# Kernel tuning notes

Measured on AMD Instinct MI355X. Metric: run time of the kernel, lower is better.

Reference implementation:

```python
import jax, jax.numpy as jnp
import numpy as np

B, S, D, H, DFF = 2, 2048, 1024, 16, 4096
HD = D // H
EPS = 1e-5


def setup_inputs() -> dict:
    key = jax.random.key(0)
    ks = jax.random.split(key, 8)
    s = lambda fan_in: 1.0 / np.sqrt(fan_in)
    return {
        "x": jax.random.normal(ks[0], (B, S, D), jnp.float32),
        "ln1_g": jnp.ones((D,), jnp.float32),
        "ln1_b": jnp.zeros((D,), jnp.float32),
        "Wq": jax.random.normal(ks[1], (D, D), jnp.float32) * s(D),
        "Wk": jax.random.normal(ks[2], (D, D), jnp.float32) * s(D),
        "Wv": jax.random.normal(ks[3], (D, D), jnp.float32) * s(D),
        "Wo": jax.random.normal(ks[4], (D, D), jnp.float32) * s(D),
        "bo": jnp.zeros((D,), jnp.float32),
        "ln2_g": jnp.ones((D,), jnp.float32),
        "ln2_b": jnp.zeros((D,), jnp.float32),
        "W1": jax.random.normal(ks[5], (D, DFF), jnp.float32) * s(D),
        "b1": jnp.zeros((DFF,), jnp.float32),
        "W2": jax.random.normal(ks[6], (DFF, D), jnp.float32) * s(DFF),
        "b2": jnp.zeros((D,), jnp.float32),
    }


def _layernorm(x, g, b):
    mu = jnp.mean(x, axis=-1, keepdims=True)
    var = jnp.var(x, axis=-1, keepdims=True)
    return (x - mu) * jax.lax.rsqrt(var + EPS) * g + b


def reference(x, ln1_g, ln1_b, Wq, Wk, Wv, Wo, bo, ln2_g, ln2_b, W1, b1, W2, b2):
    # --- pre-LN + causal multi-head attention + residual ---
    h = _layernorm(x, ln1_g, ln1_b)
    q = (h @ Wq).reshape(B, S, H, HD).transpose(0, 2, 1, 3)  # [B,H,S,hd]
    k = (h @ Wk).reshape(B, S, H, HD).transpose(0, 2, 1, 3)
    v = (h @ Wv).reshape(B, S, H, HD).transpose(0, 2, 1, 3)
    scores = jnp.einsum("bhqd,bhkd->bhqk", q, k) / jnp.sqrt(jnp.float32(HD))
    causal = jnp.triu(jnp.ones((S, S), bool), k=1)  # True above diagonal -> masked
    scores = jnp.where(causal, -jnp.inf, scores)
    attn = jax.nn.softmax(scores, axis=-1)  # dropout is identity at inference
    ctx = jnp.einsum("bhqk,bhkd->bhqd", attn, v)
    ctx = ctx.transpose(0, 2, 1, 3).reshape(B, S, D)
    x = x + ctx @ Wo + bo
    # --- pre-LN + MLP + residual ---
    h = _layernorm(x, ln2_g, ln2_b)
    h = jax.nn.gelu(h @ W1 + b1, approximate=False)  # torch nn.GELU default = exact
    x = x + h @ W2 + b2
    return x
```

## Files before the change

kernel.cpp:

```cpp
#include <hip/hip_runtime.h>
#include <hip/hip_bf16.h>
#include <math.h>

using bf16 = __hip_bfloat16;
typedef short bf16x8 __attribute__((ext_vector_type(8)));
typedef float f32x4 __attribute__((ext_vector_type(4)));

static constexpr int B = 2, S = 2048, D = 1024, H = 16, HD = 64, DFF = 4096;
static constexpr int NR = B * S;
static constexpr int DQ = 3072;
static constexpr float EPS = 1e-5f;

__device__ __forceinline__ bf16 f2b(float v) { return __float2bfloat16(v); }

__device__ __forceinline__ float gelu_exact(float v) {
    const float u = v * 0.70710678118654752f;
    const float au = fabsf(u);
    const float t = __builtin_amdgcn_rcpf(1.0f + 0.3275911f * au);
    float poly = 1.061405429f;
    poly = poly * t - 1.453152027f;
    poly = poly * t + 1.421413741f;
    poly = poly * t - 0.284496736f;
    poly = poly * t + 0.254829592f;
    poly = poly * t;
    const float ea = 1.0f - poly * __expf(-u * u);
    return 0.5f * v * (1.0f + copysignf(ea, u));
}

typedef __attribute__((address_space(1))) const void* gp1_t;
typedef __attribute__((address_space(3))) void* sp3_t;
__device__ __forceinline__ void gld_lds16(const bf16* g, bf16* l) {
    __builtin_amdgcn_global_load_lds((gp1_t)(const void*)g, (sp3_t)(void*)l, 16, 0, 0);
}

__device__ __forceinline__ void convT_body(const float* __restrict__ src,
                                           bf16* __restrict__ dst,
                                           int K, int N, int k0, int n0, int tid) {
    __shared__ float tile[64][65];
    const int r = tid >> 4, c = (tid & 15) * 4;
#pragma unroll
    for (int rr = 0; rr < 64; rr += 16) {
        float4 v = *(const float4*)&src[(size_t)(k0 + r + rr) * N + n0 + c];
        tile[r + rr][c] = v.x; tile[r + rr][c + 1] = v.y;
        tile[r + rr][c + 2] = v.z; tile[r + rr][c + 3] = v.w;
    }
    __syncthreads();
    const int n = tid >> 2, ks = (tid & 3) * 16;
    union { bf16 h[16]; int4 v2[2]; } o;
#pragma unroll
    for (int i = 0; i < 16; ++i) o.h[i] = f2b(tile[ks + i][n]);
    bf16* dp = &dst[(size_t)(n0 + n) * K + k0 + ks];
    *(int4*)dp = o.v2[0];
    *(int4*)(dp + 8) = o.v2[1];
}

__global__ __launch_bounds__(256) void convT_kernel(const float* __restrict__ src,
                                                    bf16* __restrict__ dst,
                                                    int K, int N) {
    convT_body(src, dst, K, N, blockIdx.x * 64, blockIdx.y * 64, threadIdx.x);
}

__global__ __launch_bounds__(256) void convT6_kernel(const float* __restrict__ Wq,
                                                     const float* __restrict__ Wk,
                                                     const float* __restrict__ Wv,
                                                     const float* __restrict__ Wo,
                                                     const float* __restrict__ W2,
                                                     const float* __restrict__ W1,
                                                     bf16* __restrict__ WqkvT,
                                                     bf16* __restrict__ WoT,
                                                     bf16* __restrict__ W2T,
                                                     bf16* __restrict__ W1T) {
    const int bid = blockIdx.x;
    const float* src;
    bf16* dst;
    int K, N, bx, by;
    if (bid < 768) {
        const int j = bid >> 8, r = bid & 255;
        src = (j == 0) ? Wq : ((j == 1) ? Wk : Wv);
        dst = WqkvT + (size_t)j * D * D;
        K = D; N = D; bx = r & 15; by = r >> 4;
    } else if (bid < 1024) {
        const int r = bid - 768;
        src = Wo; dst = WoT; K = D; N = D; bx = r & 15; by = r >> 4;
    } else if (bid < 2048) {
        const int r = bid - 1024;
        src = W2; dst = W2T; K = DFF; N = D; bx = r & 63; by = r >> 6;
    } else {
        const int r = bid - 2048;
        src = W1; dst = W1T; K = D; N = DFF; bx = r & 15; by = r >> 4;
    }
    convT_body(src, dst, K, N, bx * 64, by * 64, threadIdx.x);
}

__global__ __launch_bounds__(256) void ln_kernel(const float* __restrict__ x,
                                                 const float* __restrict__ g,
                                                 const float* __restrict__ b,
                                                 bf16* __restrict__ out) {
    const int row = blockIdx.x;
    const int tid = threadIdx.x;
    const float4 v4 = ((const float4*)(x + (size_t)row * D))[tid];
    float v[4] = {v4.x, v4.y, v4.z, v4.w};
    float s = v[0] + v[1] + v[2] + v[3];
    float sq = v[0] * v[0] + v[1] * v[1] + v[2] * v[2] + v[3] * v[3];
#pragma unroll
    for (int off = 32; off >= 1; off >>= 1) {
        s += __shfl_xor(s, off);
        sq += __shfl_xor(sq, off);
    }
    __shared__ float ssum[4], ssq[4];
    const int wave = tid >> 6;
    if ((tid & 63) == 0) { ssum[wave] = s; ssq[wave] = sq; }
    __syncthreads();
    s = ssum[0] + ssum[1] + ssum[2] + ssum[3];
    sq = ssq[0] + ssq[1] + ssq[2] + ssq[3];
    const float mu = s * (1.0f / D);
    const float var = sq * (1.0f / D) - mu * mu;
    const float rstd = rsqrtf(var + EPS);
    bf16* orow = out + (size_t)row * D;
#pragma unroll
    for (int i = 0; i < 4; ++i) {
        const int c = tid * 4 + i;
        orow[c] = f2b((v[i] - mu) * rstd * g[c] + b[c]);
    }
}

template <int EPI, int BN, int TPB>
__global__ __launch_bounds__(256) void gemm_bt(const bf16* __restrict__ A,
                                               const bf16* __restrict__ Bt,
                                               const float* __restrict__ bias,
                                               const float* __restrict__ res,
                                               void* __restrict__ Cv,
                                               int M, int N, int K) {
    constexpr int NTW = BN / 32;
    constexpr int AHALF = 128 * 32;
    constexpr int BHALF = BN * 32;
    constexpr int ASZ = 2 * AHALF, BSZ = 2 * BHALF;
    constexpr int CST = BN + 8;
    __shared__ __align__(16) bf16 smem[2 * (ASZ + BSZ)];

    const int Mtiles = M / 128;
    const int p = blockIdx.x;
    const int tm = p % Mtiles;
    const int tn0 = (p / Mtiles) * TPB;
    const int tid = threadIdx.x;
    const int wave = tid >> 6, lane = tid & 63;
    const int wm = wave >> 1, wn = wave & 1;
    const int quad = lane >> 4, l16 = lane & 15;

    const int r4 = tid >> 2, s4 = (tid & 3) * 8;
    const size_t K64 = (size_t)64 * K;
    const int nk = K / 64;

    for (int tp = 0; tp < TPB; ++tp) {
        const int tn = tn0 + tp;
        if (tp) __syncthreads();

        f32x4 acc[4][NTW];
#pragma unroll
        for (int i = 0; i < 4; ++i)
#pragma unroll
            for (int j = 0; j < NTW; ++j) acc[i][j] = (f32x4){0.f, 0.f, 0.f, 0.f};

        const bf16* Ap = A + (size_t)(tm * 128 + r4) * K + s4;
        const bf16* Bp = Bt + (size_t)(tn * BN + r4) * K + s4;

        gld_lds16(Ap, smem + tid * 8);
        gld_lds16(Ap + K64, smem + (256 + tid) * 8);
        gld_lds16(Ap + 32, smem + (512 + tid) * 8);
        gld_lds16(Ap + K64 + 32, smem + (768 + tid) * 8);
        gld_lds16(Bp, smem + 2 * ASZ + tid * 8);
        gld_lds16(Bp + 32, smem + 2 * ASZ + (256 + tid) * 8);
        Ap += 64;
        Bp += 64;

        for (int kt = 0; kt < nk; ++kt) {
            const int cur = kt & 1, nxt = cur ^ 1;
            bf16* Acur = smem + cur * ASZ;
            bf16* Bcur = smem + 2 * ASZ + cur * BSZ;
            __syncthreads();
            if (kt + 1 < nk) {
                bf16* Anxt = smem + nxt * ASZ;
                bf16* Bnxt = smem + 2 * ASZ + nxt * BSZ;
                gld_lds16(Ap, Anxt + tid * 8);
                gld_lds16(Ap + K64, Anxt + (256 + tid) * 8);
                gld_lds16(Ap + 32, Anxt + (512 + tid) * 8);
                gld_lds16(Ap + K64 + 32, Anxt + (768 + tid) * 8);
                gld_lds16(Bp, Bnxt + tid * 8);
                gld_lds16(Bp + 32, Bnxt + (256 + tid) * 8);
                Ap += 64;
                Bp += 64;
            }

#pragma unroll
            for (int ks = 0; ks < 2; ++ks) {
                const bf16* Ah = Acur + ks * AHALF;
                const bf16* Bh = Bcur + ks * BHALF;
                bf16x8 aF[4], bF[NTW];
#pragma unroll
                for (int mt = 0; mt < 4; ++mt)
                    aF[mt] = *(const bf16x8*)(Ah + (wm * 64 + mt * 16 + l16) * 32 + quad * 8);
#pragma unroll
                for (int nt = 0; nt < NTW; ++nt)
                    bF[nt] = *(const bf16x8*)(Bh + (wn * (BN / 2) + nt * 16 + l16) * 32 + quad * 8);
#pragma unroll
                for (int mt = 0; mt < 4; ++mt)
#pragma unroll
                    for (int nt = 0; nt < NTW; ++nt)
                        acc[mt][nt] = __builtin_amdgcn_mfma_f32_16x16x32_bf16(
                            aF[mt], bF[nt], acc[mt][nt], 0, 0, 0);
            }
        }

        if constexpr (EPI == 1) {
#pragma unroll
            for (int nt = 0; nt < NTW; ++nt) {
                const int col = tn * BN + wn * (BN / 2) + nt * 16 + l16;
                const float bv = bias[col];
#pragma unroll
                for (int mt = 0; mt < 4; ++mt) {
                    const int row0 = tm * 128 + wm * 64 + mt * 16 + quad * 4;
#pragma unroll
                    for (int j = 0; j < 4; ++j) {
                        const size_t idx = (size_t)(row0 + j) * N + col;
                        ((float*)Cv)[idx] = acc[mt][nt][j] + bv + res[idx];
                    }
                }
            }
        } else {
            bf16* C = (bf16*)Cv;
            __syncthreads();
#pragma unroll
            for (int nt = 0; nt < NTW; ++nt) {
                const int ccol = wn * (BN / 2) + nt * 16 + l16;
                float bv = 0.f;
                if (EPI == 2) bv = bias[tn * BN + ccol];
#pragma unroll
                for (int mt = 0; mt < 4; ++mt) {
                    const int r0 = wm * 64 + mt * 16 + quad * 4;
#pragma unroll
                    for (int j = 0; j < 4; ++j) {
                        float v = acc[mt][nt][j];
                        if (EPI == 2) v = gelu_exact(v + bv);
                        smem[(r0 + j) * CST + ccol] = f2b(v);
                    }
                }
            }
            __syncthreads();
            bf16* crow = C + (size_t)(tm * 128) * N + tn * BN;
#pragma unroll
            for (int i = 0; i < BN / 16; ++i) {
                const int gid = i * 256 + tid;
                const int row = gid / (BN / 8), c8 = gid % (BN / 8);
                const int4 val = *(const int4*)(smem + row * CST + c8 * 8);
                *(int4*)(crow + (size_t)row * N + c8 * 8) = val;
            }
        }
    }
}

__global__ __launch_bounds__(256) void fattn_kernel(const bf16* __restrict__ QKV,
                                                    bf16* __restrict__ ctx) {
    const int id = blockIdx.x;
    const int bh = id & 31;
    const int k = id >> 5;
    const int t = (k < 16) ? 31 - k : k - 16;
    const int b = bh >> 4, h = bh & (H - 1);
    const int tid = threadIdx.x;
    const int wave = tid >> 6, lane = tid & 63;
    const int quad = lane >> 4, l16 = lane & 15;
    const bf16* Qp = QKV + (size_t)b * S * DQ + h * HD;
    const bf16* Kp = Qp + D;
    const bf16* Vp = Qp + 2 * D;

    __shared__ __align__(16) bf16 Ks[2][64 * 64];
    __shared__ __align__(16) bf16 Vt[2][64][72];

    const int keyA = tid >> 3;
    const int sA = (keyA & 3) | ((keyA >> 1) & 4);
    const int dsA = ((tid & 7) ^ sA) * 8;
    const size_t K32 = (size_t)32 * DQ;

    const int q0 = t * 64;
    const bf16* qg = Qp + (size_t)(q0 + wave * 16 + l16) * DQ + quad * 8;
    union U8 { bf16 h[8]; bf16x8 v; };
    U8 uq0, uq1;
    uq0.v = *(const bf16x8*)(qg);
    uq1.v = *(const bf16x8*)(qg + 32);
#pragma unroll
    for (int i = 0; i < 8; ++i) {
        uq0.h[i] = f2b(__bfloat162float(uq0.h[i]) * 0.125f);
        uq1.h[i] = f2b(__bfloat162float(uq1.h[i]) * 0.125f);
    }
    const bf16x8 aQ0 = uq0.v;
    const bf16x8 aQ1 = uq1.v;

    const int kb = (l16 >> 2) * 8 + (l16 & 3);
    const int sQ = (l16 & 3) | (((l16 >> 2) & 1) << 2);
    const int ofs0 = kb * 64 + ((quad ^ sQ) * 8);
    const int ofs1 = kb * 64 + (((4 + quad) ^ sQ) * 8);

    f32x4 O[4];
#pragma unroll
    for (int nt = 0; nt < 4; ++nt) O[nt] = (f32x4){0.f, 0.f, 0.f, 0.f};
    float rowm = -3.0e38f, rowl = 0.f;

    gld_lds16(Kp + (size_t)keyA * DQ + dsA, Ks[0] + tid * 8);
    gld_lds16(Kp + K32 + (size_t)keyA * DQ + dsA, Ks[0] + (256 + tid) * 8);
    {
        const bf16* vg = Vp + (size_t)lane * DQ + wave * 16;
        U8 u0, u1;
        u0.v = *(const bf16x8*)vg;
        u1.v = *(const bf16x8*)(vg + 8);
#pragma unroll
        for (int i = 0; i < 8; ++i) {
            Vt[0][wave * 16 + i][lane] = u0.h[i];
            Vt[0][wave * 16 + 8 + i][lane] = u1.h[i];
        }
    }

    const int nch = t + 1;
    for (int c = 0; c < nch; ++c) {
        const int cur = c & 1, nxt = cur ^ 1;
        __syncthreads();
        U8 u0, u1;
        if (c + 1 < nch) {
            const bf16* kg = Kp + (size_t)((c + 1) * 64 + keyA) * DQ + dsA;
            gld_lds16(kg, Ks[nxt] + tid * 8);
            gld_lds16(kg + K32, Ks[nxt] + (256 + tid) * 8);
            const bf16* vg = Vp + (size_t)((c + 1) * 64 + lane) * DQ + wave * 16;
            u0.v = *(const bf16x8*)vg;
            u1.v = *(const bf16x8*)(vg + 8);
        }

        f32x4 sc[4];
        __builtin_amdgcn_s_setprio(1);
#pragma unroll
        for (int m = 0; m < 4; ++m) {
            const bf16* kr = Ks[cur] + (m & 1) * 256 + (m >> 1) * 2048;
            const bf16x8 bK0 = *(const bf16x8*)(kr + ofs0);
            const bf16x8 bK1 = *(const bf16x8*)(kr + ofs1);
            f32x4 z = (f32x4){0.f, 0.f, 0.f, 0.f};
            z = __builtin_amdgcn_mfma_f32_16x16x32_bf16(bK0, aQ0, z, 0, 0, 0);
            z = __builtin_amdgcn_mfma_f32_16x16x32_bf16(bK1, aQ1, z, 0, 0, 0);
            sc[m] = z;
        }
        __builtin_amdgcn_s_setprio(0);
        if (c == nch - 1) {
            const int qloc = wave * 16 + l16;
#pragma unroll
            for (int m = 0; m < 4; ++m) {
                const int kk = quad * 8 + (m & 1) * 4 + (m >> 1) * 32;
#pragma unroll
                for (int j = 0; j < 4; ++j)
                    if (kk + j > qloc) sc[m][j] = -3.0e38f;
            }
        }
        f32x4 mv;
#pragma unroll
        for (int j = 0; j < 4; ++j)
            mv[j] = fmaxf(fmaxf(sc[0][j], sc[1][j]), fmaxf(sc[2][j], sc[3][j]));
        float mx = fmaxf(fmaxf(mv[0], mv[1]), fmaxf(mv[2], mv[3]));
        mx = fmaxf(mx, __shfl_xor(mx, 16));
        mx = fmaxf(mx, __shfl_xor(mx, 32));
        if (__any(mx > rowm + 8.0f)) {
            const float mn = fmaxf(rowm, mx);
            const float alq = __expf(rowm - mn);
            rowm = mn;
            rowl *= alq;
#pragma unroll
            for (int nt = 0; nt < 4; ++nt)
#pragma unroll
                for (int j = 0; j < 4; ++j) O[nt][j] *= alq;
        }
        float rs = 0.f;
#pragma unroll
        for (int m = 0; m < 4; ++m)
#pragma unroll
            for (int j = 0; j < 4; ++j) {
                sc[m][j] = __expf(sc[m][j] - rowm);
                rs += sc[m][j];
            }
        rs += __shfl_xor(rs, 16);
        rs += __shfl_xor(rs, 32);
        rowl += rs;

        U8 p0, p1;
#pragma unroll
        for (int j = 0; j < 4; ++j) {
            p0.h[j]     = f2b(sc[0][j]);
            p0.h[4 + j] = f2b(sc[1][j]);
            p1.h[j]     = f2b(sc[2][j]);
            p1.h[4 + j] = f2b(sc[3][j]);
        }
        __builtin_amdgcn_s_setprio(1);
#pragma unroll
        for (int nt = 0; nt < 4; ++nt) {
            const bf16x8 bV0 = *(const bf16x8*)&Vt[cur][nt * 16 + l16][quad * 8];
            const bf16x8 bV1 = *(const bf16x8*)&Vt[cur][nt * 16 + l16][32 + quad * 8];
            O[nt] = __builtin_amdgcn_mfma_f32_16x16x32_bf16(bV0, p0.v, O[nt], 0, 0, 0);
            O[nt] = __builtin_amdgcn_mfma_f32_16x16x32_bf16(bV1, p1.v, O[nt], 0, 0, 0);
        }
        __builtin_amdgcn_s_setprio(0);
        if (c + 1 < nch) {
#pragma unroll
            for (int i = 0; i < 8; ++i) {
                Vt[nxt][wave * 16 + i][lane] = u0.h[i];
                Vt[nxt][wave * 16 + 8 + i][lane] = u1.h[i];
            }
        }
    }

    const float rlq = 1.0f / rowl;
    bf16* crow = ctx + (size_t)b * S * D + h * HD + (size_t)(q0 + wave * 16 + l16) * D;
#pragma unroll
    for (int nt = 0; nt < 4; ++nt) {
        union { bf16 h[4]; int2 v; } o;
#pragma unroll
        for (int j = 0; j < 4; ++j) o.h[j] = f2b(O[nt][j] * rlq);
        *(int2*)(crow + nt * 16 + quad * 4) = o.v;
    }
}

extern "C" void kernel_launch(void* const* d_in, const int* in_sizes, int n_in,
                              void* d_out, int out_size, void* d_ws, size_t ws_size,
                              hipStream_t stream) {
    const float* x     = (const float*)d_in[0];
    const float* ln1_g = (const float*)d_in[1];
    const float* ln1_b = (const float*)d_in[2];
    const float* Wq    = (const float*)d_in[3];
    const float* Wk    = (const float*)d_in[4];
    const float* Wv    = (const float*)d_in[5];
    const float* Wo    = (const float*)d_in[6];
    const float* bo    = (const float*)d_in[7];
    const float* ln2_g = (const float*)d_in[8];
    const float* ln2_b = (const float*)d_in[9];
    const float* W1    = (const float*)d_in[10];
    const float* b1    = (const float*)d_in[11];
    const float* W2    = (const float*)d_in[12];
    const float* b2    = (const float*)d_in[13];
    float* out = (float*)d_out;

    char* ws = (char*)d_ws;
    const size_t MB = (size_t)1 << 20;
    const bool wide = ws_size >= 72 * MB;
    bf16* h     = (bf16*)(ws + 0 * MB);
    bf16* QKVb  = (bf16*)(ws + 8 * MB);
    bf16* hff   = (bf16*)(ws + 8 * MB);
    bf16* ctx   = (bf16*)(ws + 32 * MB);
    bf16* h2    = (bf16*)(ws + 40 * MB);
    bf16* WqkvT = (bf16*)(ws + 48 * MB);
    bf16* WoT   = (bf16*)(ws + 54 * MB);
    bf16* W2T   = (bf16*)(ws + 56 * MB);
    bf16* W1T   = wide ? (bf16*)(ws + 64 * MB) : (bf16*)(ws + 0 * MB);

    convT6_kernel<<<wide ? 3072 : 2048, 256, 0, stream>>>(
        Wq, Wk, Wv, Wo, W2, W1, WqkvT, WoT, W2T, W1T);
    ln_kernel<<<NR, 256, 0, stream>>>(x, ln1_g, ln1_b, h);
    gemm_bt<0, 64, 1><<<(NR / 128) * (DQ / 64), 256, 0, stream>>>(
        h, WqkvT, nullptr, nullptr, QKVb, NR, DQ, D);
    if (!wide) convT_kernel<<<dim3(16, 64), 256, 0, stream>>>(W1, W1T, D, DFF);
    fattn_kernel<<<dim3((S / 64) * B * H), 256, 0, stream>>>(QKVb, ctx);
    gemm_bt<1, 64, 1><<<(NR / 128) * (D / 64), 256, 0, stream>>>(
        ctx, WoT, bo, x, out, NR, D, D);
    ln_kernel<<<NR, 256, 0, stream>>>(out, ln2_g, ln2_b, h2);
    gemm_bt<2, 64, 1><<<(NR / 128) * (DFF / 64), 256, 0, stream>>>(
        h2, W1T, b1, nullptr, hff, NR, DFF, D);
    gemm_bt<1, 64, 1><<<(NR / 128) * (D / 64), 256, 0, stream>>>(
        hff, W2T, b2, out, out, NR, D, DFF);
}
```

Measured before the change: 320.0 us.

## Triple-buffer GEMM K-loop with explicit vmcnt waits and fuse LN1 into weight prep

The GEMM main loop moves from double to triple buffering in LDS, issuing loads two tiles ahead. It uses explicit s_waitcnt vmcnt/s_barrier in place of __syncthreads, which keeps more global loads in flight and hides latency. Separately, the first LayerNorm is folded into the weight-transpose prep kernel as extra blocks, removing one launch. The cost is more LDS per block, which can lower occupancy, and the hand-written waitcnt counts must match the number of async loads per stage.

```diff
diff --git a/kernel.cpp b/kernel.cpp
--- a/kernel.cpp
+++ b/kernel.cpp
@@ -60,17 +60,61 @@
     convT_body(src, dst, K, N, blockIdx.x * 64, blockIdx.y * 64, threadIdx.x);
 }
 
-__global__ __launch_bounds__(256) void convT6_kernel(const float* __restrict__ Wq,
-                                                     const float* __restrict__ Wk,
-                                                     const float* __restrict__ Wv,
-                                                     const float* __restrict__ Wo,
-                                                     const float* __restrict__ W2,
-                                                     const float* __restrict__ W1,
-                                                     bf16* __restrict__ WqkvT,
-                                                     bf16* __restrict__ WoT,
-                                                     bf16* __restrict__ W2T,
-                                                     bf16* __restrict__ W1T) {
+__device__ __forceinline__ void ln_body(const float* __restrict__ x,
+                                        const float* __restrict__ g,
+                                        const float* __restrict__ b,
+                                        bf16* __restrict__ out, int row, int tid) {
+    const float4 v4 = ((const float4*)(x + (size_t)row * D))[tid];
+    float v[4] = {v4.x, v4.y, v4.z, v4.w};
+    float s = v[0] + v[1] + v[2] + v[3];
+    float sq = v[0] * v[0] + v[1] * v[1] + v[2] * v[2] + v[3] * v[3];
+#pragma unroll
+    for (int off = 32; off >= 1; off >>= 1) {
+        s += __shfl_xor(s, off);
+        sq += __shfl_xor(sq, off);
+    }
+    __shared__ float ssum[4], ssq[4];
+    const int wave = tid >> 6;
+    if ((tid & 63) == 0) { ssum[wave] = s; ssq[wave] = sq; }
+    __syncthreads();
+    s = ssum[0] + ssum[1] + ssum[2] + ssum[3];
+    sq = ssq[0] + ssq[1] + ssq[2] + ssq[3];
+    const float mu = s * (1.0f / D);
+    const float var = sq * (1.0f / D) - mu * mu;
+    const float rstd = rsqrtf(var + EPS);
+    bf16* orow = out + (size_t)row * D;
+#pragma unroll
+    for (int i = 0; i < 4; ++i) {
+        const int c = tid * 4 + i;
+        orow[c] = f2b((v[i] - mu) * rstd * g[c] + b[c]);
+    }
+}
+
+__global__ __launch_bounds__(256) void ln_kernel(const float* __restrict__ x,
+                                                 const float* __restrict__ g,
+                                                 const float* __restrict__ b,
+                                                 bf16* __restrict__ out) {
+    ln_body(x, g, b, out, blockIdx.x, threadIdx.x);
+}
+
+__global__ __launch_bounds__(256) void prep_kernel(const float* __restrict__ Wq,
+                                                   const float* __restrict__ Wk,
+                                                   const float* __restrict__ Wv,
+                                                   const float* __restrict__ Wo,
+                                                   const float* __restrict__ W2,
+                                                   const float* __restrict__ W1,
+                                                   bf16* __restrict__ WqkvT,
+                                                   bf16* __restrict__ WoT,
+                                                   bf16* __restrict__ W2T,
+                                                   bf16* __restrict__ W1T,
+                                                   const float* __restrict__ x,
+                                                   const float* __restrict__ ln1_g,
+                                                   const float* __restrict__ ln1_b,
+                                                   bf16* __restrict__ h,
+                                                   int nW) {
     const int bid = blockIdx.x;
+    const int tid = threadIdx.x;
+    if (bid >= nW) { ln_body(x, ln1_g, ln1_b, h, bid - nW, tid); return; }
     const float* src;
     bf16* dst;
     int K, N, bx, by;
@@ -89,42 +133,10 @@
         const int r = bid - 2048;
         src = W1; dst = W1T; K = D; N = DFF; bx = r & 15; by = r >> 4;
     }
-    convT_body(src, dst, K, N, bx * 64, by * 64, threadIdx.x);
-}
-
-__global__ __launch_bounds__(256) void ln_kernel(const float* __restrict__ x,
-                                                 const float* __restrict__ g,
-                                                 const float* __restrict__ b,
-                                                 bf16* __restrict__ out) {
-    const int row = blockIdx.x;
-    const int tid = threadIdx.x;
-    const float4 v4 = ((const float4*)(x + (size_t)row * D))[tid];
-    float v[4] = {v4.x, v4.y, v4.z, v4.w};
-    float s = v[0] + v[1] + v[2] + v[3];
-    float sq = v[0] * v[0] + v[1] * v[1] + v[2] * v[2] + v[3] * v[3];
-#pragma unroll
-    for (int off = 32; off >= 1; off >>= 1) {
-        s += __shfl_xor(s, off);
-        sq += __shfl_xor(sq, off);
-    }
-    __shared__ float ssum[4], ssq[4];
-    const int wave = tid >> 6;
-    if ((tid & 63) == 0) { ssum[wave] = s; ssq[wave] = sq; }
-    __syncthreads();
-    s = ssum[0] + ssum[1] + ssum[2] + ssum[3];
-    sq = ssq[0] + ssq[1] + ssq[2] + ssq[3];
-    const float mu = s * (1.0f / D);
-    const float var = sq * (1.0f / D) - mu * mu;
-    const float rstd = rsqrtf(var + EPS);
-    bf16* orow = out + (size_t)row * D;
-#pragma unroll
-    for (int i = 0; i < 4; ++i) {
-        const int c = tid * 4 + i;
-        orow[c] = f2b((v[i] - mu) * rstd * g[c] + b[c]);
-    }
-}
-
-template <int EPI, int BN, int TPB>
+    convT_body(src, dst, K, N, bx * 64, by * 64, tid);
+}
+
+template <int EPI, int BN>
 __global__ __launch_bounds__(256) void gemm_bt(const bf16* __restrict__ A,
                                                const bf16* __restrict__ Bt,
                                                const float* __restrict__ bias,
@@ -135,13 +147,14 @@
     constexpr int AHALF = 128 * 32;
     constexpr int BHALF = BN * 32;
     constexpr int ASZ = 2 * AHALF, BSZ = 2 * BHALF;
+    constexpr int RB = ASZ + BSZ;
     constexpr int CST = BN + 8;
-    __shared__ __align__(16) bf16 smem[2 * (ASZ + BSZ)];
+    __shared__ __align__(16) bf16 smem[3 * RB];
 
     const int Mtiles = M / 128;
     const int p = blockIdx.x;
     const int tm = p % Mtiles;
-    const int tn0 = (p / Mtiles) * TPB;
+    const int tn = p / Mtiles;
     const int tid = threadIdx.x;
     const int wave = tid >> 6, lane = tid & 63;
     const int wm = wave >> 1, wn = wave & 1;
@@ -151,109 +164,111 @@
     const size_t K64 = (size_t)64 * K;
     const int nk = K / 64;
 
-    for (int tp = 0; tp < TPB; ++tp) {
-        const int tn = tn0 + tp;
-        if (tp) __syncthreads();
-
-        f32x4 acc[4][NTW];
-#pragma unroll
-        for (int i = 0; i < 4; ++i)
-#pragma unroll
-            for (int j = 0; j < NTW; ++j) acc[i][j] = (f32x4){0.f, 0.f, 0.f, 0.f};
-
-        const bf16* Ap = A + (size_t)(tm * 128 + r4) * K + s4;
-        const bf16* Bp = Bt + (size_t)(tn * BN + r4) * K + s4;
-
-        gld_lds16(Ap, smem + tid * 8);
-        gld_lds16(Ap + K64, smem + (256 + tid) * 8);
-        gld_lds16(Ap + 32, smem + (512 + tid) * 8);
-        gld_lds16(Ap + K64 + 32, smem + (768 + tid) * 8);
-        gld_lds16(Bp, smem + 2 * ASZ + tid * 8);
-        gld_lds16(Bp + 32, smem + 2 * ASZ + (256 + tid) * 8);
-        Ap += 64;
-        Bp += 64;
-
-        for (int kt = 0; kt < nk; ++kt) {
-            const int cur = kt & 1, nxt = cur ^ 1;
-            bf16* Acur = smem + cur * ASZ;
-            bf16* Bcur = smem + 2 * ASZ + cur * BSZ;
-            __syncthreads();
-            if (kt + 1 < nk) {
-                bf16* Anxt = smem + nxt * ASZ;
-                bf16* Bnxt = smem + 2 * ASZ + nxt * BSZ;
-                gld_lds16(Ap, Anxt + tid * 8);
-                gld_lds16(Ap + K64, Anxt + (256 + tid) * 8);
-                gld_lds16(Ap + 32, Anxt + (512 + tid) * 8);
-                gld_lds16(Ap + K64 + 32, Anxt + (768 + tid) * 8);
-                gld_lds16(Bp, Bnxt + tid * 8);
-                gld_lds16(Bp + 32, Bnxt + (256 + tid) * 8);
-                Ap += 64;
-                Bp += 64;
-            }
-
-#pragma unroll
-            for (int ks = 0; ks < 2; ++ks) {
-                const bf16* Ah = Acur + ks * AHALF;
-                const bf16* Bh = Bcur + ks * BHALF;
-                bf16x8 aF[4], bF[NTW];
-#pragma unroll
-                for (int mt = 0; mt < 4; ++mt)
-                    aF[mt] = *(const bf16x8*)(Ah + (wm * 64 + mt * 16 + l16) * 32 + quad * 8);
+    f32x4 acc[4][NTW];
+#pragma unroll
+    for (int i = 0; i < 4; ++i)
+#pragma unroll
+        for (int j = 0; j < NTW; ++j) acc[i][j] = (f32x4){0.f, 0.f, 0.f, 0.f};
+
+    const bf16* Ap = A + (size_t)(tm * 128 + r4) * K + s4;
+    const bf16* Bp = Bt + (size_t)(tn * BN + r4) * K + s4;
+
+    auto stage = [&](const bf16* ap, const bf16* bp, int d) {
+        bf16* base = smem + d * RB;
+        gld_lds16(ap,            base + tid * 8);
+        gld_lds16(ap + K64,      base + (256 + tid) * 8);
+        gld_lds16(ap + 32,       base + (512 + tid) * 8);
+        gld_lds16(ap + K64 + 32, base + (768 + tid) * 8);
+        gld_lds16(bp,            base + ASZ + tid * 8);
+        gld_lds16(bp + 32,       base + ASZ + (256 + tid) * 8);
+    };
+
+    stage(Ap, Bp, 0);
+    stage(Ap + 64, Bp + 64, 1);
+    Ap += 128;
+    Bp += 128;
+
+    int cur = 0;
+    for (int kt = 0; kt < nk; ++kt) {
+        if (kt + 1 < nk) {
+            asm volatile("s_waitcnt vmcnt(6) lgkmcnt(0)" ::: "memory");
+        } else {
+            asm volatile("s_waitcnt vmcnt(0) lgkmcnt(0)" ::: "memory");
+        }
+        __builtin_amdgcn_s_barrier();
+        if (kt + 2 < nk) {
+            int wb = cur + 2;
+            if (wb >= 3) wb -= 3;
+            stage(Ap, Bp, wb);
+            Ap += 64;
+            Bp += 64;
+        }
+
+        const bf16* Acur = smem + cur * RB;
+        const bf16* Bcur = Acur + ASZ;
+#pragma unroll
+        for (int ks = 0; ks < 2; ++ks) {
+            const bf16* Ah = Acur + ks * AHALF;
+            const bf16* Bh = Bcur + ks * BHALF;
+            bf16x8 aF[4], bF[NTW];
+#pragma unroll
+            for (int mt = 0; mt < 4; ++mt)
+                aF[mt] = *(const bf16x8*)(Ah + (wm * 64 + mt * 16 + l16) * 32 + quad * 8);
+#pragma unroll
+            for (int nt = 0; nt < NTW; ++nt)
+                bF[nt] = *(const bf16x8*)(Bh + (wn * (BN / 2) + nt * 16 + l16) * 32 + quad * 8);
+#pragma unroll
+            for (int mt = 0; mt < 4; ++mt)
 #pragma unroll
                 for (int nt = 0; nt < NTW; ++nt)
-                    bF[nt] = *(const bf16x8*)(Bh + (wn * (BN / 2) + nt * 16 + l16) * 32 + quad * 8);
-#pragma unroll
-                for (int mt = 0; mt < 4; ++mt)
-#pragma unroll
-                    for (int nt = 0; nt < NTW; ++nt)
-                        acc[mt][nt] = __builtin_amdgcn_mfma_f32_16x16x32_bf16(
-                            aF[mt], bF[nt], acc[mt][nt], 0, 0, 0);
-            }
-        }
-
-        if constexpr (EPI == 1) {
-#pragma unroll
-            for (int nt = 0; nt < NTW; ++nt) {
-                const int col = tn * BN + wn * (BN / 2) + nt * 16 + l16;
-                const float bv = bias[col];
-#pragma unroll
-                for (int mt = 0; mt < 4; ++mt) {
-                    const int row0 = tm * 128 + wm * 64 + mt * 16 + quad * 4;
-#pragma unroll
-                    for (int j = 0; j < 4; ++j) {
-                        const size_t idx = (size_t)(row0 + j) * N + col;
-                        ((float*)Cv)[idx] = acc[mt][nt][j] + bv + res[idx];
-                    }
+                    acc[mt][nt] = __builtin_amdgcn_mfma_f32_16x16x32_bf16(
+                        aF[mt], bF[nt], acc[mt][nt], 0, 0, 0);
+        }
+        cur = (cur + 1 == 3) ? 0 : cur + 1;
+    }
+
+    if constexpr (EPI == 1) {
+#pragma unroll
+        for (int nt = 0; nt < NTW; ++nt) {
+            const int col = tn * BN + wn * (BN / 2) + nt * 16 + l16;
+            const float bv = bias[col];
+#pragma unroll
+            for (int mt = 0; mt < 4; ++mt) {
+                const int row0 = tm * 128 + wm * 64 + mt * 16 + quad * 4;
+#pragma unroll
+                for (int j = 0; j < 4; ++j) {
+                    const size_t idx = (size_t)(row0 + j) * N + col;
+                    ((float*)Cv)[idx] = acc[mt][nt][j] + bv + res[idx];
                 }
             }
-        } else {
-            bf16* C = (bf16*)Cv;
-            __syncthreads();
-#pragma unroll
-            for (int nt = 0; nt < NTW; ++nt) {
-                const int ccol = wn * (BN / 2) + nt * 16 + l16;
-                float bv = 0.f;
-                if (EPI == 2) bv = bias[tn * BN + ccol];
-#pragma unroll
-                for (int mt = 0; mt < 4; ++mt) {
-                    const int r0 = wm * 64 + mt * 16 + quad * 4;
-#pragma unroll
-                    for (int j = 0; j < 4; ++j) {
-                        float v = acc[mt][nt][j];
-                        if (EPI == 2) v = gelu_exact(v + bv);
-                        smem[(r0 + j) * CST + ccol] = f2b(v);
-                    }
+        }
+    } else {
+        bf16* C = (bf16*)Cv;
+        __syncthreads();
+#pragma unroll
+        for (int nt = 0; nt < NTW; ++nt) {
+            const int ccol = wn * (BN / 2) + nt * 16 + l16;
+            float bv = 0.f;
+            if (EPI == 2) bv = bias[tn * BN + ccol];
+#pragma unroll
+            for (int mt = 0; mt < 4; ++mt) {
+                const int r0 = wm * 64 + mt * 16 + quad * 4;
+#pragma unroll
+                for (int j = 0; j < 4; ++j) {
+                    float v = acc[mt][nt][j];
+                    if (EPI == 2) v = gelu_exact(v + bv);
+                    smem[(r0 + j) * CST + ccol] = f2b(v);
                 }
             }
-            __syncthreads();
-            bf16* crow = C + (size_t)(tm * 128) * N + tn * BN;
-#pragma unroll
-            for (int i = 0; i < BN / 16; ++i) {
-                const int gid = i * 256 + tid;
-                const int row = gid / (BN / 8), c8 = gid % (BN / 8);
-                const int4 val = *(const int4*)(smem + row * CST + c8 * 8);
-                *(int4*)(crow + (size_t)row * N + c8 * 8) = val;
-            }
+        }
+        __syncthreads();
+        bf16* crow = C + (size_t)(tm * 128) * N + tn * BN;
+#pragma unroll
+        for (int i = 0; i < BN / 16; ++i) {
+            const int gid = i * 256 + tid;
+            const int row = gid / (BN / 8), c8 = gid % (BN / 8);
+            const int4 val = *(const int4*)(smem + row * CST + c8 * 8);
+            *(int4*)(crow + (size_t)row * N + c8 * 8) = val;
         }
     }
 }
@@ -453,18 +468,18 @@
     bf16* W2T   = (bf16*)(ws + 56 * MB);
     bf16* W1T   = wide ? (bf16*)(ws + 64 * MB) : (bf16*)(ws + 0 * MB);
 
-    convT6_kernel<<<wide ? 3072 : 2048, 256, 0, stream>>>(
-        Wq, Wk, Wv, Wo, W2, W1, WqkvT, WoT, W2T, W1T);
-    ln_kernel<<<NR, 256, 0, stream>>>(x, ln1_g, ln1_b, h);
-    gemm_bt<0, 64, 1><<<(NR / 128) * (DQ / 64), 256, 0, stream>>>(
+    const int nW = wide ? 3072 : 2048;
+    prep_kernel<<<nW + NR, 256, 0, stream>>>(
+        Wq, Wk, Wv, Wo, W2, W1, WqkvT, WoT, W2T, W1T, x, ln1_g, ln1_b, h, nW);
+    gemm_bt<0, 64><<<(NR / 128) * (DQ / 64), 256, 0, stream>>>(
         h, WqkvT, nullptr, nullptr, QKVb, NR, DQ, D);
     if (!wide) convT_kernel<<<dim3(16, 64), 256, 0, stream>>>(W1, W1T, D, DFF);
     fattn_kernel<<<dim3((S / 64) * B * H), 256, 0, stream>>>(QKVb, ctx);
-    gemm_bt<1, 64, 1><<<(NR / 128) * (D / 64), 256, 0, stream>>>(
+    gemm_bt<1, 64><<<(NR / 128) * (D / 64), 256, 0, stream>>>(
         ctx, WoT, bo, x, out, NR, D, D);
     ln_kernel<<<NR, 256, 0, stream>>>(out, ln2_g, ln2_b, h2);
-    gemm_bt<2, 64, 1><<<(NR / 128) * (DFF / 64), 256, 0, stream>>>(
+    gemm_bt<2, 64><<<(NR / 128) * (DFF / 64), 256, 0, stream>>>(
         h2, W1T, b1, nullptr, hff, NR, DFF, D);
-    gemm_bt<1, 64, 1><<<(NR / 128) * (D / 64), 256, 0, stream>>>(
+    gemm_bt<1, 64><<<(NR / 128) * (D / 64), 256, 0, stream>>>(
         hff, W2T, b2, out, out, NR, D, DFF);
 }
```

Measured after the change: 332.1 us. 3.8% more time.
